# Performance work log

Hardware: AMD Instinct MI355X
Metric: run time of the kernel (lower is better)

The kernel has to match this reference:

```python
import jax, jax.numpy as jnp
import numpy as np

D_MODEL = 1024
NUM_HEADS = 16
NUM_KV_HEADS = 4
HEAD_DIM = D_MODEL // NUM_HEADS  # 64
KV_DIM = HEAD_DIM * NUM_KV_HEADS  # 256
B, N = 2, 2048


def setup_inputs() -> dict:
    key = jax.random.key(0)
    ks = jax.random.split(key, 7)
    std = 1.0 / np.sqrt(D_MODEL)
    return {
        "x": jax.random.normal(ks[0], (B, N, D_MODEL), dtype=jnp.float32),
        "cos": jax.random.uniform(ks[1], (N, HEAD_DIM // 2), dtype=jnp.float32),
        "sin": jax.random.uniform(ks[2], (N, HEAD_DIM // 2), dtype=jnp.float32),
        "Wq": jax.random.normal(ks[3], (D_MODEL, D_MODEL), dtype=jnp.float32) * std,
        "Wk": jax.random.normal(ks[4], (D_MODEL, KV_DIM), dtype=jnp.float32) * std,
        "Wv": jax.random.normal(ks[5], (D_MODEL, KV_DIM), dtype=jnp.float32) * std,
        "Wo": jax.random.normal(ks[6], (D_MODEL, D_MODEL), dtype=jnp.float32) * std,
    }


def _rope(t, cos, sin):
    # t: [B, H, N, head_dim]; cos/sin: [N, head_dim//2]
    t1, t2 = t[..., ::2], t[..., 1::2]
    c = cos[None, None]
    s = sin[None, None]
    # NOTE: halves are concatenated (not re-interleaved), faithful to source.
    return jnp.concatenate([t1 * c - t2 * s, t1 * s + t2 * c], axis=-1)


def reference(x, cos, sin, Wq, Wk, Wv, Wo):
    b, n, d = x.shape
    scale = HEAD_DIM ** -0.5
    q = (x @ Wq).reshape(b, n, NUM_HEADS, HEAD_DIM).transpose(0, 2, 1, 3)
    k = (x @ Wk).reshape(b, n, NUM_KV_HEADS, HEAD_DIM).transpose(0, 2, 1, 3)
    v = (x @ Wv).reshape(b, n, NUM_KV_HEADS, HEAD_DIM).transpose(0, 2, 1, 3)
    q = _rope(q, cos, sin)
    k = _rope(k, cos, sin)
    num_rep = NUM_HEADS // NUM_KV_HEADS
    k = jnp.repeat(k, num_rep, axis=1)  # [b, H, n, hd]
    v = jnp.repeat(v, num_rep, axis=1)
    attn = jnp.einsum("bhqd,bhkd->bhqk", q, k) * scale
    attn = jax.nn.softmax(attn, axis=-1)
    out = jnp.einsum("bhqk,bhkd->bhqd", attn, v)
    out = out.transpose(0, 2, 1, 3).reshape(b, n, d)
    return out @ Wo
```

## Files before the change

kernel.cpp:

```cpp
#include <hip/hip_runtime.h>
#include <math.h>

#define D_MODEL 1024
#define NHEADS  16
#define NKV     4
#define HDIM    64
#define KVDIM   256
#define BB      2
#define NN      2048
#define MROWS   (BB*NN)
#define QKVN    1536
#define NTASK   (MROWS*NHEADS)
#define NSPLIT  2

typedef unsigned short ushort_t;
typedef unsigned int uint_t;
typedef float    f32x4 __attribute__((ext_vector_type(4)));
typedef _Float16 h16x8 __attribute__((ext_vector_type(8)));
typedef __fp16   fp16x2 __attribute__((ext_vector_type(2)));

#define MFMAH(A,B,C) __builtin_amdgcn_mfma_f32_16x16x32_f16((A),(B),(C),0,0,0)

#define GLDS(gp, lp) __builtin_amdgcn_global_load_lds( \
    (const __attribute__((address_space(1))) void*)(gp), \
    (__attribute__((address_space(3))) void*)(lp), 16, 0, 0)

__device__ __forceinline__ ushort_t f2h(float f) {
    _Float16 h = (_Float16)f;
    return *(ushort_t*)&h;
}
__device__ __forceinline__ float h2f(ushort_t u) {
    return (float)(*(const _Float16*)&u);
}
__device__ __forceinline__ uint_t pk2h(float a, float b) {
    fp16x2 v = __builtin_amdgcn_cvt_pkrtz(a, b);
    return *(uint_t*)&v;
}

__global__ __launch_bounds__(256)
void prep_kernel(const float* __restrict__ x, const float* __restrict__ Wq,
                 const float* __restrict__ Wk, const float* __restrict__ Wv,
                 const float* __restrict__ Wo, ushort_t* __restrict__ xb,
                 ushort_t* __restrict__ WqkvT, ushort_t* __restrict__ WoT)
{
    __shared__ float T[32][33];
    int blk = blockIdx.x;
    if (blk < 4096) {
        const int i = blk * 256 + threadIdx.x;
        float4 v = ((const float4*)x)[i];
        uint2 o;
        o.x = pk2h(v.x, v.y);
        o.y = pk2h(v.z, v.w);
        ((uint2*)xb)[i] = o;
        return;
    }
    blk -= 4096;
    const float* src; ushort_t* dst; int N, bx, by;
    if (blk < 1024)      { src = Wq; dst = WqkvT;                            N = D_MODEL; bx = blk & 31; by = blk >> 5; }
    else if (blk < 1280) { blk -= 1024; src = Wk; dst = WqkvT + (size_t)1024 * D_MODEL; N = KVDIM; bx = blk & 7; by = blk >> 3; }
    else if (blk < 1536) { blk -= 1280; src = Wv; dst = WqkvT + (size_t)1280 * D_MODEL; N = KVDIM; bx = blk & 7; by = blk >> 3; }
    else                 { blk -= 1536; src = Wo; dst = WoT;                 N = D_MODEL; bx = blk & 31; by = blk >> 5; }
    const int tx = threadIdx.x & 31, ty = threadIdx.x >> 5;
    const int n0 = bx * 32, k0 = by * 32;
#pragma unroll
    for (int i = 0; i < 4; i++)
        T[ty + i * 8][tx] = src[(size_t)(k0 + ty + i * 8) * N + n0 + tx];
    __syncthreads();
#pragma unroll
    for (int i = 0; i < 4; i++)
        dst[(size_t)(n0 + ty + i * 8) * D_MODEL + k0 + tx] = f2h(T[tx][ty + i * 8]);
}

__global__ __launch_bounds__(256)
void vtrans_kernel(const ushort_t* __restrict__ QKVh, ushort_t* __restrict__ Vt)
{
    __shared__ ushort_t T[32][34];
    const int tx = threadIdx.x & 31, ty = threadIdx.x >> 5;
    const int n0 = blockIdx.x * 32, d0 = blockIdx.y * 32, b = blockIdx.z;
#pragma unroll
    for (int i = 0; i < 4; i++)
        T[ty + i * 8][tx] =
            QKVh[(size_t)(b * NN + n0 + ty + i * 8) * QKVN + 1280 + d0 + tx];
    __syncthreads();
#pragma unroll
    for (int i = 0; i < 4; i++)
        Vt[(size_t)(b * 256 + d0 + ty + i * 8) * NN + n0 + tx] = T[tx][ty + i * 8];
}

#define NQW (MROWS*NHEADS*32)
#define NKW (MROWS*NKV*32)
__global__ __launch_bounds__(256)
void rope_kernel(const ushort_t* __restrict__ QKVh, const float* __restrict__ Cos,
                 const float* __restrict__ Sin, ushort_t* __restrict__ Qb,
                 ushort_t* __restrict__ Kb)
{
    const float SC = 0.125f * 1.44269504f;
    int idx = blockIdx.x * 256 + threadIdx.x;
    if (idx < NQW) {
        const int row = idx >> 9, rem = idx & 511;
        const int h = rem >> 5, j = rem & 31;
        const int b = row >> 11, n = row & (NN - 1);
        const uint_t pr = *(const uint_t*)&QKVh[(size_t)row * QKVN + h * 64 + 2 * j];
        const float e = h2f((ushort_t)pr), o = h2f((ushort_t)(pr >> 16));
        const float c = Cos[n * 32 + j], s = Sin[n * 32 + j];
        ushort_t* dst = Qb + ((size_t)(b * 16 + h) * NN + n) * 64;
        dst[j]      = f2h((e * c - o * s) * SC);
        dst[j + 32] = f2h((e * s + o * c) * SC);
    } else {
        const int i2 = idx - NQW;
        const int row = i2 >> 7, rem = i2 & 127;
        const int h = rem >> 5, j = rem & 31;
        const int b = row >> 11, n = row & (NN - 1);
        const uint_t pr = *(const uint_t*)&QKVh[(size_t)row * QKVN + 1024 + h * 64 + 2 * j];
        const float e = h2f((ushort_t)pr), o = h2f((ushort_t)(pr >> 16));
        const float c = Cos[n * 32 + j], s = Sin[n * 32 + j];
        ushort_t* dst = Kb + ((size_t)(b * 4 + h) * NN + n) * 64;
        dst[j]      = f2h(e * c - o * s);
        dst[j + 32] = f2h(e * s + o * c);
    }
}

__global__ __launch_bounds__(256)
void gemm_qkv(const ushort_t* __restrict__ A, const ushort_t* __restrict__ Bt,
              ushort_t* __restrict__ C, int M, int N, int K)
{
    __shared__ ushort_t As[2][128 * 32];
    __shared__ ushort_t Bs[2][64 * 32];

    const int tid  = threadIdx.x;
    const int wave = tid >> 6, lane = tid & 63;
    const int quad = lane >> 4, l16 = lane & 15;
    const int rowBase = blockIdx.y * 128, colBase = blockIdx.x * 64;
    const int wm = (wave >> 1) * 64, wn = (wave & 1) * 32;

    f32x4 acc[4][2];
    const f32x4 zz = {0.f, 0.f, 0.f, 0.f};
#pragma unroll
    for (int i = 0; i < 4; i++)
#pragma unroll
        for (int j = 0; j < 2; j++) acc[i][j] = zz;

    const int sr = wave * 32 + (lane >> 2);
    const int sc = ((lane & 3) ^ ((lane >> 3) & 3)) * 8;
    const ushort_t* Ag0 = A + (size_t)(rowBase + sr) * K + sc;
    const ushort_t* Ag1 = A + (size_t)(rowBase + sr + 16) * K + sc;
    const int segA0 = (wave * 2 + 0) * 512, segA1 = (wave * 2 + 1) * 512;
    const int br = wave * 16 + (lane >> 2);
    const ushort_t* Bg0 = Bt + (size_t)(colBase + br) * K + sc;
    const int segB = wave * 512;

    const int fcol = (quad ^ ((l16 >> 1) & 3)) * 8;

    GLDS(Ag0, &As[0][segA0]);
    GLDS(Ag1, &As[0][segA1]);
    GLDS(Bg0, &Bs[0][segB]);

    for (int k0 = 0; k0 < K; k0 += 32) {
        const int cur = (k0 >> 5) & 1, nxt = cur ^ 1;
        __syncthreads();
        if (k0 + 32 < K) {
            GLDS(Ag0 + k0 + 32, &As[nxt][segA0]);
            GLDS(Ag1 + k0 + 32, &As[nxt][segA1]);
            GLDS(Bg0 + k0 + 32, &Bs[nxt][segB]);
        }

        h16x8 af[4], bf[2];
#pragma unroll
        for (int mt = 0; mt < 4; mt++)
            af[mt] = *(const h16x8*)&As[cur][(wm + mt * 16 + l16) * 32 + fcol];
#pragma unroll
        for (int nt = 0; nt < 2; nt++)
            bf[nt] = *(const h16x8*)&Bs[cur][(wn + nt * 16 + l16) * 32 + fcol];
#pragma unroll
        for (int mt = 0; mt < 4; mt++)
#pragma unroll
            for (int nt = 0; nt < 2; nt++)
                acc[mt][nt] = MFMAH(af[mt], bf[nt], acc[mt][nt]);
    }

#pragma unroll
    for (int mt = 0; mt < 4; mt++)
#pragma unroll
        for (int nt = 0; nt < 2; nt++) {
            const int row = rowBase + wm + mt * 16 + quad * 4;
            const int col = colBase + wn + nt * 16 + l16;
#pragma unroll
            for (int r = 0; r < 4; r++)
                C[(size_t)(row + r) * N + col] = f2h(acc[mt][nt][r]);
        }
}

__global__ __launch_bounds__(256)
void attn_mfma(const ushort_t* __restrict__ Qb, const ushort_t* __restrict__ Kb,
               const ushort_t* __restrict__ Vt, ushort_t* __restrict__ Pnum,
               float* __restrict__ Pl)
{
    const int qt = blockIdx.x, h = blockIdx.y;
    const int b = blockIdx.z >> 1, chunk = blockIdx.z & 1;
    const int kvh = h >> 2;
    const int tid = threadIdx.x;
    const int wave = tid >> 6, lane = tid & 63;
    const int quad = lane >> 4, l16 = lane & 15;

    __shared__ ushort_t Ks[64][72];
    __shared__ ushort_t Vs[64][72];
    __shared__ ushort_t Ps[4][16 * 72];
    ushort_t* ps = &Ps[wave][0];

    const int row0 = qt * 256 + wave * 64;
    h16x8 qf[4][2];
#pragma unroll
    for (int mt = 0; mt < 4; mt++) {
        const ushort_t* qp =
            Qb + ((size_t)(b * 16 + h) * NN + row0 + mt * 16 + l16) * 64 + quad * 8;
        qf[mt][0] = *(const h16x8*)qp;
        qf[mt][1] = *(const h16x8*)(qp + 32);
    }

    const ushort_t* kbase = Kb + (size_t)(b * 4 + kvh) * NN * 64;
    const ushort_t* vbase = Vt + (size_t)(b * 256 + kvh * 64) * NN;
    const int key_lo = chunk * (NN / NSPLIT);
    const int rot = (qt + ((h & 3) << 2)) & 15;

    const int srow = tid >> 2, sseg = (tid & 3) * 8;

    const f32x4 zz = {0.f, 0.f, 0.f, 0.f};
    f32x4 o[4][4];
#pragma unroll
    for (int mt = 0; mt < 4; mt++)
#pragma unroll
        for (int dt = 0; dt < 4; dt++) o[mt][dt] = zz;
    float lacc[4] = {0.f, 0.f, 0.f, 0.f};

    int key0 = key_lo + rot * 64;
    const ushort_t* kp0 = kbase + (size_t)(key0 + srow) * 64 + sseg;
    const ushort_t* vp0 = vbase + (size_t)srow * NN + key0 + sseg;
    uint4 kreg0 = *(const uint4*)kp0;
    uint4 kreg1 = *(const uint4*)(kp0 + 32);
    uint4 vreg0 = *(const uint4*)vp0;
    uint4 vreg1 = *(const uint4*)(vp0 + 32);

    for (int t = 0; t < 16; t++) {
        __syncthreads();
        *(uint4*)&Ks[srow][sseg]      = kreg0;
        *(uint4*)&Ks[srow][sseg + 32] = kreg1;
        *(uint4*)&Vs[srow][sseg]      = vreg0;
        *(uint4*)&Vs[srow][sseg + 32] = vreg1;
        __syncthreads();

        if (t < 15) {
            const int kn = key_lo + ((rot + t + 1) & 15) * 64;
            const ushort_t* kpn = kbase + (size_t)(kn + srow) * 64 + sseg;
            const ushort_t* vpn = vbase + (size_t)srow * NN + kn + sseg;
            kreg0 = *(const uint4*)kpn;
            kreg1 = *(const uint4*)(kpn + 32);
            vreg0 = *(const uint4*)vpn;
            vreg1 = *(const uint4*)(vpn + 32);
        }

        uint2 pkreg[4][4];
#pragma unroll
        for (int kt = 0; kt < 4; kt++) {
            h16x8 kf0 = *(const h16x8*)&Ks[kt * 16 + l16][quad * 8];
            h16x8 kf1 = *(const h16x8*)&Ks[kt * 16 + l16][32 + quad * 8];
#pragma unroll
            for (int mt = 0; mt < 4; mt++) {
                f32x4 st = MFMAH(kf0, qf[mt][0], zz);
                st = MFMAH(kf1, qf[mt][1], st);
                const float p0 = exp2f(st[0]);
                const float p1 = exp2f(st[1]);
                const float p2 = exp2f(st[2]);
                const float p3 = exp2f(st[3]);
                lacc[mt] += (p0 + p1) + (p2 + p3);
                pkreg[kt][mt].x = pk2h(p0, p1);
                pkreg[kt][mt].y = pk2h(p2, p3);
            }
        }

        h16x8 vf[4][2];
#pragma unroll
        for (int dt = 0; dt < 4; dt++) {
            vf[dt][0] = *(const h16x8*)&Vs[dt * 16 + l16][quad * 8];
            vf[dt][1] = *(const h16x8*)&Vs[dt * 16 + l16][32 + quad * 8];
        }
#pragma unroll
        for (int mt = 0; mt < 4; mt++) {
#pragma unroll
            for (int kt = 0; kt < 4; kt++)
                *(uint2*)&ps[l16 * 72 + kt * 16 + quad * 4] = pkreg[kt][mt];
            h16x8 pa0 = *(const h16x8*)&ps[l16 * 72 + quad * 8];
            h16x8 pa1 = *(const h16x8*)&ps[l16 * 72 + 32 + quad * 8];
#pragma unroll
            for (int dt = 0; dt < 4; dt++) {
                o[mt][dt] = MFMAH(vf[dt][0], pa0, o[mt][dt]);
                o[mt][dt] = MFMAH(vf[dt][1], pa1, o[mt][dt]);
            }
        }
    }

#pragma unroll
    for (int mt = 0; mt < 4; mt++) {
        lacc[mt] += __shfl_xor(lacc[mt], 16, 64);
        lacc[mt] += __shfl_xor(lacc[mt], 32, 64);
    }

    const size_t task0 = (size_t)(b * 16 + h) * NN + row0;
    ushort_t* np = Pnum + ((size_t)chunk * NTASK + task0) * 64;
#pragma unroll
    for (int mt = 0; mt < 4; mt++) {
        const float inv = 1.0f / lacc[mt];
#pragma unroll
        for (int dt = 0; dt < 4; dt++) {
            f32x4 v = o[mt][dt];
            uint2 pk;
            pk.x = pk2h(v[0] * inv, v[1] * inv);
            pk.y = pk2h(v[2] * inv, v[3] * inv);
            *(uint2*)&np[(size_t)(mt * 16 + l16) * 64 + dt * 16 + quad * 4] = pk;
        }
        if (quad == 0)
            Pl[(size_t)chunk * NTASK + task0 + mt * 16 + l16] = lacc[mt];
    }
}

__global__ __launch_bounds__(256)
void gemm_wo(const ushort_t* __restrict__ Pnum, const float* __restrict__ Pl,
             const ushort_t* __restrict__ WoT, float* __restrict__ C)
{
    __shared__ ushort_t As[2][128 * 40];
    __shared__ ushort_t Bs[2][64 * 32];

    const int tid  = threadIdx.x;
    const int wave = tid >> 6, lane = tid & 63;
    const int quad = lane >> 4, l16 = lane & 15;
    const int rowBase = blockIdx.y * 128, colBase = blockIdx.x * 64;
    const int wm = (wave >> 1) * 64, wn = (wave & 1) * 32;

    f32x4 acc[4][2];
    const f32x4 zz = {0.f, 0.f, 0.f, 0.f};
#pragma unroll
    for (int i = 0; i < 4; i++)
#pragma unroll
        for (int j = 0; j < 2; j++) acc[i][j] = zz;

    const int r0 = tid >> 2;
    const int c8 = (tid & 3) * 8;
    const int bB = rowBase >> 11;
    const int n0 = (rowBase & (NN - 1)) + r0;

    const int br = wave * 16 + (lane >> 2);
    const int sc = ((lane & 3) ^ ((lane >> 3) & 3)) * 8;
    const ushort_t* Bg0 = WoT + (size_t)(colBase + br) * D_MODEL + sc;
    const int segB = wave * 512;
    const int fcol = (quad ^ ((l16 >> 1) & 3)) * 8;

    uint4 a0c0, a0c1, a1c0, a1c1;
    float l00, l01, l10, l11;
#define PREFA(k0) { \
        const int h_ = (k0) >> 6; \
        const int d_ = ((k0) & 63) + c8; \
        const size_t t0_ = ((size_t)(bB * 16 + h_) << 11) + n0; \
        const size_t t1_ = t0_ + 64; \
        a0c0 = *(const uint4*)&Pnum[t0_ * 64 + d_]; \
        a0c1 = *(const uint4*)&Pnum[((size_t)NTASK + t0_) * 64 + d_]; \
        a1c0 = *(const uint4*)&Pnum[t1_ * 64 + d_]; \
        a1c1 = *(const uint4*)&Pnum[((size_t)NTASK + t1_) * 64 + d_]; \
        l00 = Pl[t0_]; l01 = Pl[NTASK + t0_]; \
        l10 = Pl[t1_]; l11 = Pl[NTASK + t1_]; \
    }

    PREFA(0);
    GLDS(Bg0, &Bs[0][segB]);

    for (int k0 = 0; k0 < D_MODEL; k0 += 32) {
        const int cur = (k0 >> 5) & 1, nxt = cur ^ 1;
        __syncthreads();

        {
            const float i0 = 1.f / (l00 + l01), w00 = l00 * i0, w01 = l01 * i0;
            const float i1 = 1.f / (l10 + l11), w10 = l10 * i1, w11 = l11 * i1;
            uint4 o0, o1;
            const uint_t* p0 = (const uint_t*)&a0c0;
            const uint_t* p1 = (const uint_t*)&a0c1;
            const uint_t* q0 = (const uint_t*)&a1c0;
            const uint_t* q1 = (const uint_t*)&a1c1;
            uint_t* po = (uint_t*)&o0;
            uint_t* qo = (uint_t*)&o1;
#pragma unroll
            for (int j = 0; j < 4; j++) {
                fp16x2 u = *(const fp16x2*)&p0[j];
                fp16x2 v = *(const fp16x2*)&p1[j];
                po[j] = pk2h(w00 * (float)u.x + w01 * (float)v.x,
                             w00 * (float)u.y + w01 * (float)v.y);
                fp16x2 s = *(const fp16x2*)&q0[j];
                fp16x2 r = *(const fp16x2*)&q1[j];
                qo[j] = pk2h(w10 * (float)s.x + w11 * (float)r.x,
                             w10 * (float)s.y + w11 * (float)r.y);
            }
            *(uint4*)&As[cur][r0 * 40 + c8]        = o0;
            *(uint4*)&As[cur][(r0 + 64) * 40 + c8] = o1;
        }
        __syncthreads();

        if (k0 + 32 < D_MODEL) {
            GLDS(Bg0 + k0 + 32, &Bs[nxt][segB]);
            PREFA(k0 + 32);
        }

        h16x8 af[4], bf[2];
#pragma unroll
        for (int mt = 0; mt < 4; mt++)
            af[mt] = *(const h16x8*)&As[cur][(wm + mt * 16 + l16) * 40 + quad * 8];
#pragma unroll
        for (int nt = 0; nt < 2; nt++)
            bf[nt] = *(const h16x8*)&Bs[cur][(wn + nt * 16 + l16) * 32 + fcol];
#pragma unroll
        for (int mt = 0; mt < 4; mt++)
#pragma unroll
            for (int nt = 0; nt < 2; nt++)
                acc[mt][nt] = MFMAH(af[mt], bf[nt], acc[mt][nt]);
    }
#undef PREFA

#pragma unroll
    for (int mt = 0; mt < 4; mt++)
#pragma unroll
        for (int nt = 0; nt < 2; nt++) {
            const int row = rowBase + wm + mt * 16 + quad * 4;
            const int col = colBase + wn + nt * 16 + l16;
#pragma unroll
            for (int r = 0; r < 4; r++)
                C[(size_t)(row + r) * D_MODEL + col] = acc[mt][nt][r];
        }
}

extern "C" void kernel_launch(void* const* d_in, const int* in_sizes, int n_in,
                              void* d_out, int out_size, void* d_ws, size_t ws_size,
                              hipStream_t stream)
{
    const float* x    = (const float*)d_in[0];
    const float* cosp = (const float*)d_in[1];
    const float* sinp = (const float*)d_in[2];
    const float* Wq   = (const float*)d_in[3];
    const float* Wk   = (const float*)d_in[4];
    const float* Wv   = (const float*)d_in[5];
    const float* Wo   = (const float*)d_in[6];

    char* w = (char*)d_ws;
    ushort_t* xb     = (ushort_t*)w;                       w += (size_t)MROWS * D_MODEL * 2;
    ushort_t* WqkvT  = (ushort_t*)w;                       w += (size_t)QKVN * D_MODEL * 2;
    ushort_t* WoT    = (ushort_t*)w;                       w += (size_t)D_MODEL * D_MODEL * 2;
    ushort_t* QKVh   = (ushort_t*)w;                       w += (size_t)MROWS * QKVN * 2;
    ushort_t* Qbuf   = (ushort_t*)w;                       w += (size_t)MROWS * D_MODEL * 2;
    ushort_t* Kbuf   = (ushort_t*)w;                       w += (size_t)MROWS * KVDIM * 2;
    ushort_t* Vt     = (ushort_t*)w;                       w += (size_t)MROWS * KVDIM * 2;
    ushort_t* Pnum   = (ushort_t*)w;                       w += (size_t)NSPLIT * NTASK * 64 * 2;
    float*    Pl     = (float*)w;

    prep_kernel<<<6656, 256, 0, stream>>>(x, Wq, Wk, Wv, Wo, xb, WqkvT, WoT);

    gemm_qkv<<<dim3(QKVN / 64, MROWS / 128), 256, 0, stream>>>(
        xb, WqkvT, QKVh, MROWS, QKVN, D_MODEL);

    rope_kernel<<<(NQW + NKW) / 256, 256, 0, stream>>>(QKVh, cosp, sinp, Qbuf, Kbuf);
    vtrans_kernel<<<dim3(NN / 32, KVDIM / 32, BB), 256, 0, stream>>>(QKVh, Vt);

    attn_mfma<<<dim3(NN / 256, NHEADS, BB * NSPLIT), 256, 0, stream>>>(
        Qbuf, Kbuf, Vt, Pnum, Pl);

    gemm_wo<<<dim3(D_MODEL / 64, MROWS / 128), 256, 0, stream>>>(
        Pnum, Pl, WoT, (float*)d_out);
}
```

Before: 213.1 us.

## Double-buffer K/V tiles, batch P staging, compute row sums via MFMA

Double-buffers the K and V shared-memory tiles so each iteration needs one barrier instead of two. Gives each wave four separate P staging buffers, so all P tiles are written before any are read back. Replaces the scalar exp row-sum accumulation and final shuffles with extra MFMAs against a ones vector. This adds LDS usage and two more MFMAs per tile. The sum is now taken from fp16-rounded P, which matches the numerator.

```diff
diff --git a/kernel.cpp b/kernel.cpp
--- a/kernel.cpp
+++ b/kernel.cpp
@@ -202,10 +202,9 @@
     const int wave = tid >> 6, lane = tid & 63;
     const int quad = lane >> 4, l16 = lane & 15;
 
-    __shared__ ushort_t Ks[64][72];
-    __shared__ ushort_t Vs[64][72];
-    __shared__ ushort_t Ps[4][16 * 72];
-    ushort_t* ps = &Ps[wave][0];
+    __shared__ ushort_t Ks[2][64][72];
+    __shared__ ushort_t Vs[2][64][72];
+    __shared__ ushort_t Ps[4][4][16 * 72];
 
     const int row0 = qt * 256 + wave * 64;
     h16x8 qf[4][2];
@@ -217,12 +216,18 @@
         qf[mt][1] = *(const h16x8*)(qp + 32);
     }
 
+    h16x8 ones;
+#pragma unroll
+    for (int i = 0; i < 8; i++) ones[i] = (_Float16)1.0f;
+
     const ushort_t* kbase = Kb + (size_t)(b * 4 + kvh) * NN * 64;
     const ushort_t* vbase = Vt + (size_t)(b * 256 + kvh * 64) * NN;
     const int key_lo = chunk * (NN / NSPLIT);
     const int rot = (qt + ((h & 3) << 2)) & 15;
 
     const int srow = tid >> 2, sseg = (tid & 3) * 8;
+    const ushort_t* kp_lane = kbase + (size_t)srow * 64 + sseg;
+    const ushort_t* vp_lane = vbase + (size_t)srow * NN + sseg;
 
     const f32x4 zz = {0.f, 0.f, 0.f, 0.f};
     f32x4 o[4][4];
@@ -230,39 +235,37 @@
     for (int mt = 0; mt < 4; mt++)
 #pragma unroll
         for (int dt = 0; dt < 4; dt++) o[mt][dt] = zz;
-    float lacc[4] = {0.f, 0.f, 0.f, 0.f};
-
-    int key0 = key_lo + rot * 64;
-    const ushort_t* kp0 = kbase + (size_t)(key0 + srow) * 64 + sseg;
-    const ushort_t* vp0 = vbase + (size_t)srow * NN + key0 + sseg;
-    uint4 kreg0 = *(const uint4*)kp0;
-    uint4 kreg1 = *(const uint4*)(kp0 + 32);
-    uint4 vreg0 = *(const uint4*)vp0;
-    uint4 vreg1 = *(const uint4*)(vp0 + 32);
+    f32x4 lsum[4];
+#pragma unroll
+    for (int mt = 0; mt < 4; mt++) lsum[mt] = zz;
+
+    const int key0 = key_lo + rot * 64;
+    uint4 kreg0 = *(const uint4*)(kp_lane + (size_t)key0 * 64);
+    uint4 kreg1 = *(const uint4*)(kp_lane + (size_t)key0 * 64 + 32);
+    uint4 vreg0 = *(const uint4*)(vp_lane + key0);
+    uint4 vreg1 = *(const uint4*)(vp_lane + key0 + 32);
 
     for (int t = 0; t < 16; t++) {
-        __syncthreads();
-        *(uint4*)&Ks[srow][sseg]      = kreg0;
-        *(uint4*)&Ks[srow][sseg + 32] = kreg1;
-        *(uint4*)&Vs[srow][sseg]      = vreg0;
-        *(uint4*)&Vs[srow][sseg + 32] = vreg1;
-        __syncthreads();
+        const int cur = t & 1;
+        *(uint4*)&Ks[cur][srow][sseg]      = kreg0;
+        *(uint4*)&Ks[cur][srow][sseg + 32] = kreg1;
+        *(uint4*)&Vs[cur][srow][sseg]      = vreg0;
+        *(uint4*)&Vs[cur][srow][sseg + 32] = vreg1;
 
         if (t < 15) {
             const int kn = key_lo + ((rot + t + 1) & 15) * 64;
-            const ushort_t* kpn = kbase + (size_t)(kn + srow) * 64 + sseg;
-            const ushort_t* vpn = vbase + (size_t)srow * NN + kn + sseg;
-            kreg0 = *(const uint4*)kpn;
-            kreg1 = *(const uint4*)(kpn + 32);
-            vreg0 = *(const uint4*)vpn;
-            vreg1 = *(const uint4*)(vpn + 32);
-        }
+            kreg0 = *(const uint4*)(kp_lane + (size_t)kn * 64);
+            kreg1 = *(const uint4*)(kp_lane + (size_t)kn * 64 + 32);
+            vreg0 = *(const uint4*)(vp_lane + kn);
+            vreg1 = *(const uint4*)(vp_lane + kn + 32);
+        }
+        __syncthreads();
 
         uint2 pkreg[4][4];
 #pragma unroll
         for (int kt = 0; kt < 4; kt++) {
-            h16x8 kf0 = *(const h16x8*)&Ks[kt * 16 + l16][quad * 8];
-            h16x8 kf1 = *(const h16x8*)&Ks[kt * 16 + l16][32 + quad * 8];
+            h16x8 kf0 = *(const h16x8*)&Ks[cur][kt * 16 + l16][quad * 8];
+            h16x8 kf1 = *(const h16x8*)&Ks[cur][kt * 16 + l16][32 + quad * 8];
 #pragma unroll
             for (int mt = 0; mt < 4; mt++) {
                 f32x4 st = MFMAH(kf0, qf[mt][0], zz);
@@ -271,7 +274,6 @@
                 const float p1 = exp2f(st[1]);
                 const float p2 = exp2f(st[2]);
                 const float p3 = exp2f(st[3]);
-                lacc[mt] += (p0 + p1) + (p2 + p3);
                 pkreg[kt][mt].x = pk2h(p0, p1);
                 pkreg[kt][mt].y = pk2h(p2, p3);
             }
@@ -280,35 +282,34 @@
         h16x8 vf[4][2];
 #pragma unroll
         for (int dt = 0; dt < 4; dt++) {
-            vf[dt][0] = *(const h16x8*)&Vs[dt * 16 + l16][quad * 8];
-            vf[dt][1] = *(const h16x8*)&Vs[dt * 16 + l16][32 + quad * 8];
-        }
+            vf[dt][0] = *(const h16x8*)&Vs[cur][dt * 16 + l16][quad * 8];
+            vf[dt][1] = *(const h16x8*)&Vs[cur][dt * 16 + l16][32 + quad * 8];
+        }
+#pragma unroll
+        for (int mt = 0; mt < 4; mt++)
+#pragma unroll
+            for (int kt = 0; kt < 4; kt++)
+                *(uint2*)&Ps[wave][mt][l16 * 72 + kt * 16 + quad * 4] = pkreg[kt][mt];
 #pragma unroll
         for (int mt = 0; mt < 4; mt++) {
-#pragma unroll
-            for (int kt = 0; kt < 4; kt++)
-                *(uint2*)&ps[l16 * 72 + kt * 16 + quad * 4] = pkreg[kt][mt];
-            h16x8 pa0 = *(const h16x8*)&ps[l16 * 72 + quad * 8];
-            h16x8 pa1 = *(const h16x8*)&ps[l16 * 72 + 32 + quad * 8];
+            h16x8 pa0 = *(const h16x8*)&Ps[wave][mt][l16 * 72 + quad * 8];
+            h16x8 pa1 = *(const h16x8*)&Ps[wave][mt][l16 * 72 + 32 + quad * 8];
 #pragma unroll
             for (int dt = 0; dt < 4; dt++) {
                 o[mt][dt] = MFMAH(vf[dt][0], pa0, o[mt][dt]);
                 o[mt][dt] = MFMAH(vf[dt][1], pa1, o[mt][dt]);
             }
-        }
-    }
-
-#pragma unroll
-    for (int mt = 0; mt < 4; mt++) {
-        lacc[mt] += __shfl_xor(lacc[mt], 16, 64);
-        lacc[mt] += __shfl_xor(lacc[mt], 32, 64);
+            lsum[mt] = MFMAH(ones, pa0, lsum[mt]);
+            lsum[mt] = MFMAH(ones, pa1, lsum[mt]);
+        }
     }
 
     const size_t task0 = (size_t)(b * 16 + h) * NN + row0;
     ushort_t* np = Pnum + ((size_t)chunk * NTASK + task0) * 64;
 #pragma unroll
     for (int mt = 0; mt < 4; mt++) {
-        const float inv = 1.0f / lacc[mt];
+        const float lt = lsum[mt][0];
+        const float inv = 1.0f / lt;
 #pragma unroll
         for (int dt = 0; dt < 4; dt++) {
             f32x4 v = o[mt][dt];
@@ -318,7 +319,7 @@
             *(uint2*)&np[(size_t)(mt * 16 + l16) * 64 + dt * 16 + quad * 4] = pk;
         }
         if (quad == 0)
-            Pl[(size_t)chunk * NTASK + task0 + mt * 16 + l16] = lacc[mt];
+            Pl[(size_t)chunk * NTASK + task0 + mt * 16 + l16] = lt;
     }
 }
 
```

New measurement: 232.4 us. 9.1% more time.

## Feed P to PV MFMA directly from registers via 16x16x16 instructions

Applied to the files above, without the earlier changes.

The PV product now uses the 16x16x16 f16 MFMA, whose operand layout matches the register layout of the QK^T output. The probability tile can therefore be fed straight from registers instead of being written to LDS and read back. This removes the per-wave P shared-memory buffer and its store/load round trip, and interleaves the PV MFMAs with each key subtile. In exchange it issues twice as many smaller MFMAs, which have lower throughput per instruction, and does more narrow V reads from LDS.

```diff
diff --git a/kernel.cpp b/kernel.cpp
--- a/kernel.cpp
+++ b/kernel.cpp
@@ -17,9 +17,11 @@
 typedef unsigned int uint_t;
 typedef float    f32x4 __attribute__((ext_vector_type(4)));
 typedef _Float16 h16x8 __attribute__((ext_vector_type(8)));
+typedef _Float16 h16x4 __attribute__((ext_vector_type(4)));
 typedef __fp16   fp16x2 __attribute__((ext_vector_type(2)));
 
-#define MFMAH(A,B,C) __builtin_amdgcn_mfma_f32_16x16x32_f16((A),(B),(C),0,0,0)
+#define MFMAH(A,B,C)  __builtin_amdgcn_mfma_f32_16x16x32_f16((A),(B),(C),0,0,0)
+#define MFMA16(A,B,C) __builtin_amdgcn_mfma_f32_16x16x16f16((A),(B),(C),0,0,0)
 
 #define GLDS(gp, lp) __builtin_amdgcn_global_load_lds( \
     (const __attribute__((address_space(1))) void*)(gp), \
@@ -204,8 +206,6 @@
 
     __shared__ ushort_t Ks[64][72];
     __shared__ ushort_t Vs[64][72];
-    __shared__ ushort_t Ps[4][16 * 72];
-    ushort_t* ps = &Ps[wave][0];
 
     const int row0 = qt * 256 + wave * 64;
     h16x8 qf[4][2];
@@ -258,11 +258,16 @@
             vreg1 = *(const uint4*)(vpn + 32);
         }
 
-        uint2 pkreg[4][4];
 #pragma unroll
         for (int kt = 0; kt < 4; kt++) {
             h16x8 kf0 = *(const h16x8*)&Ks[kt * 16 + l16][quad * 8];
             h16x8 kf1 = *(const h16x8*)&Ks[kt * 16 + l16][32 + quad * 8];
+            h16x4 va[4];
+#pragma unroll
+            for (int dt = 0; dt < 4; dt++)
+                va[dt] = *(const h16x4*)&Vs[dt * 16 + l16][kt * 16 + quad * 4];
+
+            uint2 pb[4];
 #pragma unroll
             for (int mt = 0; mt < 4; mt++) {
                 f32x4 st = MFMAH(kf0, qf[mt][0], zz);
@@ -272,28 +277,15 @@
                 const float p2 = exp2f(st[2]);
                 const float p3 = exp2f(st[3]);
                 lacc[mt] += (p0 + p1) + (p2 + p3);
-                pkreg[kt][mt].x = pk2h(p0, p1);
-                pkreg[kt][mt].y = pk2h(p2, p3);
+                pb[mt].x = pk2h(p0, p1);
+                pb[mt].y = pk2h(p2, p3);
             }
-        }
-
-        h16x8 vf[4][2];
-#pragma unroll
-        for (int dt = 0; dt < 4; dt++) {
-            vf[dt][0] = *(const h16x8*)&Vs[dt * 16 + l16][quad * 8];
-            vf[dt][1] = *(const h16x8*)&Vs[dt * 16 + l16][32 + quad * 8];
-        }
-#pragma unroll
-        for (int mt = 0; mt < 4; mt++) {
-#pragma unroll
-            for (int kt = 0; kt < 4; kt++)
-                *(uint2*)&ps[l16 * 72 + kt * 16 + quad * 4] = pkreg[kt][mt];
-            h16x8 pa0 = *(const h16x8*)&ps[l16 * 72 + quad * 8];
-            h16x8 pa1 = *(const h16x8*)&ps[l16 * 72 + 32 + quad * 8];
-#pragma unroll
-            for (int dt = 0; dt < 4; dt++) {
-                o[mt][dt] = MFMAH(vf[dt][0], pa0, o[mt][dt]);
-                o[mt][dt] = MFMAH(vf[dt][1], pa1, o[mt][dt]);
+#pragma unroll
+            for (int mt = 0; mt < 4; mt++) {
+                const h16x4 pbv = *(const h16x4*)&pb[mt];
+#pragma unroll
+                for (int dt = 0; dt < 4; dt++)
+                    o[mt][dt] = MFMA16(va[dt], pbv, o[mt][dt]);
             }
         }
     }
```

Result: no change. 211.3 us (-0.8%).
